# Performance work log

Hardware: AMD Instinct MI355X
Metric: run time of the kernel (lower is better)

The kernel has to match this reference:

```python
import jax, jax.numpy as jnp
import numpy as np

N, P, H = 4096, 128, 4
E = P // H           # per-head embed dim (=32)
NSEG = 32            # number of distinct position segments
NEG = -1e30          # mask fill (safe finite -inf)


def setup_inputs() -> dict:
    key = jax.random.key(0)
    ks = jax.random.split(key, 8)
    s = 1.0 / np.sqrt(P)
    return {
        "inp": jax.random.normal(ks[0], (N, P), jnp.float32),
        "pos": jax.random.randint(ks[1], (N,), 0, NSEG, jnp.int32),
        "Wq": jax.random.normal(ks[2], (P, P), jnp.float32) * s,
        "bq": jnp.zeros((P,), jnp.float32),
        "Wk": jax.random.normal(ks[3], (P, P), jnp.float32) * s,
        "bk": jnp.zeros((P,), jnp.float32),
        "Wv": jax.random.normal(ks[4], (P, P), jnp.float32) * s,
        "bv": jnp.zeros((P,), jnp.float32),
    }


def reference(inp, pos, Wq, bq, Wk, bk, Wv, bv):
    # Per-segment multi-head self-attention. The TF while_loop gathers rows of
    # each unique `pos` value, runs attention within that segment, and scatters
    # results back to the original row order. This is mathematically identical
    # to full attention with a same-segment mask (softmax restricted to keys
    # in the same segment), which is the vectorized form here.
    n = inp.shape[0]

    def heads(x, W, b):
        # (n, p) -> (h, n, e), matching rearrange 'n (h e) -> h n e'
        y = x @ W + b
        return y.reshape(n, H, E).transpose(1, 0, 2)

    q = heads(inp, Wq, bq)
    k = heads(inp, Wk, bk)
    v = heads(inp, Wv, bv)

    score = jnp.einsum('hne,hme->hnm', q, k) / np.sqrt(E).astype(np.float32)
    same_seg = (pos[:, None] == pos[None, :])[None, :, :]      # (1, n, n)
    score = jnp.where(same_seg, score, NEG)
    weight = jax.nn.softmax(score, axis=-1)                    # (h, n, n)
    out = jnp.einsum('hnm,hme->hne', weight, v)                # (h, n, e)
    # rearrange 'h n e -> n (h e)'
    return out.transpose(1, 0, 2).reshape(n, P)
```

## Files before the change

kernel.cpp:

```cpp
#include <hip/hip_runtime.h>
#include <hip/hip_bf16.h>
#include <math.h>

#define N 4096
#define P 128
#define H 4
#define E 32
#define NSEG 32
#define TPB 256
#define PROJ_TASKS 192

#define VSTRIDE 264
#define NEGF -3.0e38f

typedef __attribute__((ext_vector_type(8))) short bf16x8;
typedef __attribute__((ext_vector_type(4))) float f32x4;
typedef unsigned short u16;

__device__ __forceinline__ u16 f2b(float x) {
    __hip_bfloat16 b = __float2bfloat16(x);
    return *(u16*)&b;
}

__device__ __forceinline__ void sort_phase(const int* __restrict__ pos,
                                           int* __restrict__ seg_rows,
                                           int* __restrict__ seg_off,
                                           int* sm, int t) {
    int* cnt = sm;
    int* cur = sm + NSEG;
    int* off = sm + 2 * NSEG;
    if (t < NSEG) cnt[t] = 0;
    __syncthreads();
    for (int i = t; i < N; i += TPB) atomicAdd(&cnt[pos[i]], 1);
    __syncthreads();
    if (t == 0) {
        int s = 0;
        for (int k = 0; k < NSEG; ++k) { off[k] = s; s += cnt[k]; }
        off[NSEG] = s;
    }
    __syncthreads();
    if (t <= NSEG) seg_off[t] = off[t];
    if (t < NSEG) cur[t] = off[t];
    __syncthreads();
    for (int i = t; i < N; i += TPB) {
        int r = atomicAdd(&cur[pos[i]], 1);
        seg_rows[r] = i;
    }
}

__device__ __forceinline__ void proj_phase(int task,
                                           const float* __restrict__ x,
                                           const float* __restrict__ Wq, const float* __restrict__ bq,
                                           const float* __restrict__ Wk, const float* __restrict__ bk,
                                           const float* __restrict__ Wv, const float* __restrict__ bv,
                                           u16* __restrict__ Q, u16* __restrict__ Ko, u16* __restrict__ Vo,
                                           float* sm, int t) {
    float* Xl = sm;
    float* Wl = sm + 8192;

    const int mat = task >> 6;
    const int r0  = (task & 63) * 64;
    const float* W = (mat == 0) ? Wq : (mat == 1) ? Wk : Wv;
    const float* b = (mat == 0) ? bq : (mat == 1) ? bk : bv;
    u16* y         = (mat == 0) ? Q  : (mat == 1) ? Ko : Vo;

    for (int i = t * 4; i < 64 * 128; i += TPB * 4) {
        *(float4*)(Xl + i) = *(const float4*)(x + (size_t)r0 * 128 + i);
    }

    const int tc = t & 31;
    const int tr = t >> 5;

    float4 bb = *(const float4*)(b + tc * 4);
    float4 acc[8];
#pragma unroll
    for (int r = 0; r < 8; ++r) acc[r] = bb;

    for (int kc = 0; kc < 128; kc += 32) {
        __syncthreads();
        for (int i = t * 4; i < 32 * 128; i += TPB * 4) {
            *(float4*)(Wl + i) = *(const float4*)(W + (size_t)kc * 128 + i);
        }
        __syncthreads();
#pragma unroll
        for (int k0 = 0; k0 < 32; k0 += 4) {
            float4 w0 = *(float4*)&Wl[(k0 + 0) * 128 + tc * 4];
            float4 w1 = *(float4*)&Wl[(k0 + 1) * 128 + tc * 4];
            float4 w2 = *(float4*)&Wl[(k0 + 2) * 128 + tc * 4];
            float4 w3 = *(float4*)&Wl[(k0 + 3) * 128 + tc * 4];
#pragma unroll
            for (int r = 0; r < 8; ++r) {
                float4 xv = *(float4*)&Xl[(tr * 8 + r) * 128 + kc + k0];
                acc[r].x = fmaf(xv.x, w0.x, acc[r].x);
                acc[r].y = fmaf(xv.x, w0.y, acc[r].y);
                acc[r].z = fmaf(xv.x, w0.z, acc[r].z);
                acc[r].w = fmaf(xv.x, w0.w, acc[r].w);
                acc[r].x = fmaf(xv.y, w1.x, acc[r].x);
                acc[r].y = fmaf(xv.y, w1.y, acc[r].y);
                acc[r].z = fmaf(xv.y, w1.z, acc[r].z);
                acc[r].w = fmaf(xv.y, w1.w, acc[r].w);
                acc[r].x = fmaf(xv.z, w2.x, acc[r].x);
                acc[r].y = fmaf(xv.z, w2.y, acc[r].y);
                acc[r].z = fmaf(xv.z, w2.z, acc[r].z);
                acc[r].w = fmaf(xv.z, w2.w, acc[r].w);
                acc[r].x = fmaf(xv.w, w3.x, acc[r].x);
                acc[r].y = fmaf(xv.w, w3.y, acc[r].y);
                acc[r].z = fmaf(xv.w, w3.z, acc[r].z);
                acc[r].w = fmaf(xv.w, w3.w, acc[r].w);
            }
        }
    }

#pragma unroll
    for (int r = 0; r < 8; ++r) {
        ushort4 st;
        st.x = f2b(acc[r].x); st.y = f2b(acc[r].y);
        st.z = f2b(acc[r].z); st.w = f2b(acc[r].w);
        *(ushort4*)(y + (size_t)(r0 + tr * 8 + r) * 128 + tc * 4) = st;
    }
}

__global__ __launch_bounds__(TPB) void sort_proj_kernel(
        const float* __restrict__ inp, const int* __restrict__ pos,
        const float* __restrict__ Wq, const float* __restrict__ bq,
        const float* __restrict__ Wk, const float* __restrict__ bk,
        const float* __restrict__ Wv, const float* __restrict__ bv,
        u16* __restrict__ Q, u16* __restrict__ Kb, u16* __restrict__ Vb,
        int* __restrict__ seg_rows, int* __restrict__ seg_off) {
    __shared__ __align__(16) float sm[12288];
    const int b = blockIdx.x;
    const int t = threadIdx.x;
    if (b == 0) {
        sort_phase(pos, seg_rows, seg_off, (int*)sm, t);
    } else {
        proj_phase(b - 1, inp, Wq, bq, Wk, bk, Wv, bv, Q, Kb, Vb, sm, t);
    }
}

template <int KT>
__device__ __forceinline__ void attn_body(int beg, int len, int h, int z,
                                          const u16* __restrict__ Qb,
                                          const u16* __restrict__ Kb,
                                          const u16* __restrict__ Vb,
                                          const int* __restrict__ seg_rows,
                                          float* __restrict__ out,
                                          u16* __restrict__ smu,
                                          int t, int w, int col, int quad) {
    const float scale = 0.17677669529663687f;
    u16* Vt = smu;
    u16* Ps = smu + (32 + w * 16) * VSTRIDE;

#pragma unroll
    for (int ii = 0; ii < KT / 4; ++ii) {
        const int idx = ii * TPB + t;
        const int key = idx >> 2, c = idx & 3;
        bf16x8 v = {0, 0, 0, 0, 0, 0, 0, 0};
        if (key < len)
            v = *(const bf16x8*)(Vb + (size_t)seg_rows[beg + key] * 128 + h * 32 + c * 8);
#pragma unroll
        for (int j = 0; j < 8; ++j)
            Vt[(c * 8 + j) * VSTRIDE + key] = (u16)v[j];
    }

    const int tt = z * 4 + w;
    const bool have = (tt * 16 < len);
    float lrow[4];

    if (have) {
        const int qi = beg + min(tt * 16 + col, len - 1);
        const bf16x8 qa = *(const bf16x8*)(Qb + (size_t)seg_rows[qi] * 128 + h * 32 + quad * 8);

        int krow[KT];
#pragma unroll
        for (int kt = 0; kt < KT; ++kt)
            krow[kt] = seg_rows[beg + min(kt * 16 + col, len - 1)];

        f32x4 S[KT];
#pragma unroll
        for (int kt = 0; kt < KT; ++kt) {
            const bf16x8 kb = *(const bf16x8*)(Kb + (size_t)krow[kt] * 128 + h * 32 + quad * 8);
            f32x4 c = {0.f, 0.f, 0.f, 0.f};
            S[kt] = __builtin_amdgcn_mfma_f32_16x16x32_bf16(qa, kb, c, 0, 0, 0);
        }

        float mrow[4] = {NEGF, NEGF, NEGF, NEGF};
#pragma unroll
        for (int kt = 0; kt < KT; ++kt) {
            const bool kvalid = (kt * 16 + col) < len;
#pragma unroll
            for (int r = 0; r < 4; ++r) {
                const float sc = kvalid ? S[kt][r] * scale : NEGF;
                S[kt][r] = sc;
                mrow[r] = fmaxf(mrow[r], sc);
            }
        }
#pragma unroll
        for (int d = 1; d < 16; d <<= 1) {
#pragma unroll
            for (int r = 0; r < 4; ++r)
                mrow[r] = fmaxf(mrow[r], __shfl_xor(mrow[r], d));
        }
        lrow[0] = lrow[1] = lrow[2] = lrow[3] = 0.f;
#pragma unroll
        for (int kt = 0; kt < KT; ++kt) {
#pragma unroll
            for (int r = 0; r < 4; ++r) {
                const float p = __expf(S[kt][r] - mrow[r]);
                S[kt][r] = p;
                lrow[r] += p;
            }
        }
#pragma unroll
        for (int d = 1; d < 16; d <<= 1) {
#pragma unroll
            for (int r = 0; r < 4; ++r)
                lrow[r] += __shfl_xor(lrow[r], d);
        }
#pragma unroll
        for (int kt = 0; kt < KT; ++kt) {
#pragma unroll
            for (int r = 0; r < 4; ++r)
                Ps[(quad * 4 + r) * VSTRIDE + kt * 16 + col] = f2b(S[kt][r]);
        }
    }

    __syncthreads();

    if (have) {
        f32x4 o0 = {0.f, 0.f, 0.f, 0.f}, o1 = {0.f, 0.f, 0.f, 0.f};
#pragma unroll
        for (int kg = 0; kg < KT / 2; ++kg) {
            const bf16x8 pa = *(const bf16x8*)(Ps + col * VSTRIDE + kg * 32 + quad * 8);
            const bf16x8 v0 = *(const bf16x8*)(Vt + col * VSTRIDE + kg * 32 + quad * 8);
            const bf16x8 v1 = *(const bf16x8*)(Vt + (16 + col) * VSTRIDE + kg * 32 + quad * 8);
            o0 = __builtin_amdgcn_mfma_f32_16x16x32_bf16(pa, v0, o0, 0, 0, 0);
            o1 = __builtin_amdgcn_mfma_f32_16x16x32_bf16(pa, v1, o1, 0, 0, 0);
        }
#pragma unroll
        for (int r = 0; r < 4; ++r) {
            const int qloc = tt * 16 + quad * 4 + r;
            if (qloc < len) {
                const int orow = seg_rows[beg + qloc];
                const float inv = 1.0f / lrow[r];
                float* op = out + (size_t)orow * 128 + h * 32;
                op[col]      = o0[r] * inv;
                op[16 + col] = o1[r] * inv;
            }
        }
    }
}

__global__ __launch_bounds__(TPB) void attn_kernel(const u16* __restrict__ Qb,
                                                   const u16* __restrict__ Kb,
                                                   const u16* __restrict__ Vb,
                                                   const int* __restrict__ seg_rows,
                                                   const int* __restrict__ seg_off,
                                                   float* __restrict__ out) {
    __shared__ u16 smu[VSTRIDE * (32 + 4 * 16)];

    const int s = blockIdx.x, h = blockIdx.y, z = blockIdx.z;
    const int beg = seg_off[s];
    const int len = seg_off[s + 1] - beg;
    if (z * 64 >= len) return;
    const int t = threadIdx.x, w = t >> 6;
    const int lane = t & 63, col = lane & 15, quad = lane >> 4;

    if (len <= 128)
        attn_body<8>(beg, len, h, z, Qb, Kb, Vb, seg_rows, out, smu, t, w, col, quad);
    else
        attn_body<16>(beg, len, h, z, Qb, Kb, Vb, seg_rows, out, smu, t, w, col, quad);
}

extern "C" void kernel_launch(void* const* d_in, const int* in_sizes, int n_in,
                              void* d_out, int out_size, void* d_ws, size_t ws_size,
                              hipStream_t stream) {
    const float* inp = (const float*)d_in[0];
    const int*   pos = (const int*)d_in[1];
    const float* Wq  = (const float*)d_in[2];
    const float* bq  = (const float*)d_in[3];
    const float* Wk  = (const float*)d_in[4];
    const float* bk  = (const float*)d_in[5];
    const float* Wv  = (const float*)d_in[6];
    const float* bv  = (const float*)d_in[7];
    float* out = (float*)d_out;

    u16* Qb = (u16*)d_ws;
    u16* Kb = Qb + (size_t)N * 128;
    u16* Vb = Kb + (size_t)N * 128;
    int* seg_rows = (int*)(Vb + (size_t)N * 128);
    int* seg_off  = seg_rows + N;

    sort_proj_kernel<<<1 + PROJ_TASKS, TPB, 0, stream>>>(
        inp, pos, Wq, bq, Wk, bk, Wv, bv, Qb, Kb, Vb, seg_rows, seg_off);

    attn_kernel<<<dim3(NSEG, H, 4), TPB, 0, stream>>>(
        Qb, Kb, Vb, seg_rows, seg_off, out);
}
```

Measured before the change: 90.90 us.

## Replace whole-segment attention with per-wave online-softmax over 128-key chunks

The attention kernel now has each wave loop over keys in chunks of 128 using an online softmax (running max, sum and rescaled accumulators). Previously the block loaded the whole segment's V into shared memory and switched between 8-tile and 16-tile template paths. Each wave now stages its own copy of V and P in a private LDS region, so the block-wide __syncthreads is gone and a wave only waits on itself. The cost is that every wave reloads and transposes the same V chunk, adding redundant global and LDS traffic. It also adds the rescale arithmetic for segments longer than 128 keys.

New measurement: 93.91 us. 3.3% more time.

```diff
diff --git a/kernel.cpp b/kernel.cpp
--- a/kernel.cpp
+++ b/kernel.cpp
@@ -10,7 +10,7 @@
 #define TPB 256
 #define PROJ_TASKS 192
 
-#define VSTRIDE 264
+#define VS2 136
 #define NEGF -3.0e38f
 
 typedef __attribute__((ext_vector_type(8))) short bf16x8;
@@ -137,138 +137,135 @@
     }
 }
 
-template <int KT>
-__device__ __forceinline__ void attn_body(int beg, int len, int h, int z,
-                                          const u16* __restrict__ Qb,
-                                          const u16* __restrict__ Kb,
-                                          const u16* __restrict__ Vb,
-                                          const int* __restrict__ seg_rows,
-                                          float* __restrict__ out,
-                                          u16* __restrict__ smu,
-                                          int t, int w, int col, int quad) {
-    const float scale = 0.17677669529663687f;
-    u16* Vt = smu;
-    u16* Ps = smu + (32 + w * 16) * VSTRIDE;
-
-#pragma unroll
-    for (int ii = 0; ii < KT / 4; ++ii) {
-        const int idx = ii * TPB + t;
-        const int key = idx >> 2, c = idx & 3;
-        bf16x8 v = {0, 0, 0, 0, 0, 0, 0, 0};
-        if (key < len)
-            v = *(const bf16x8*)(Vb + (size_t)seg_rows[beg + key] * 128 + h * 32 + c * 8);
-#pragma unroll
-        for (int j = 0; j < 8; ++j)
-            Vt[(c * 8 + j) * VSTRIDE + key] = (u16)v[j];
-    }
-
-    const int tt = z * 4 + w;
-    const bool have = (tt * 16 < len);
-    float lrow[4];
-
-    if (have) {
-        const int qi = beg + min(tt * 16 + col, len - 1);
-        const bf16x8 qa = *(const bf16x8*)(Qb + (size_t)seg_rows[qi] * 128 + h * 32 + quad * 8);
-
-        int krow[KT];
-#pragma unroll
-        for (int kt = 0; kt < KT; ++kt)
-            krow[kt] = seg_rows[beg + min(kt * 16 + col, len - 1)];
-
-        f32x4 S[KT];
-#pragma unroll
-        for (int kt = 0; kt < KT; ++kt) {
-            const bf16x8 kb = *(const bf16x8*)(Kb + (size_t)krow[kt] * 128 + h * 32 + quad * 8);
-            f32x4 c = {0.f, 0.f, 0.f, 0.f};
-            S[kt] = __builtin_amdgcn_mfma_f32_16x16x32_bf16(qa, kb, c, 0, 0, 0);
-        }
-
-        float mrow[4] = {NEGF, NEGF, NEGF, NEGF};
-#pragma unroll
-        for (int kt = 0; kt < KT; ++kt) {
-            const bool kvalid = (kt * 16 + col) < len;
-#pragma unroll
-            for (int r = 0; r < 4; ++r) {
-                const float sc = kvalid ? S[kt][r] * scale : NEGF;
-                S[kt][r] = sc;
-                mrow[r] = fmaxf(mrow[r], sc);
-            }
-        }
-#pragma unroll
-        for (int d = 1; d < 16; d <<= 1) {
-#pragma unroll
-            for (int r = 0; r < 4; ++r)
-                mrow[r] = fmaxf(mrow[r], __shfl_xor(mrow[r], d));
-        }
-        lrow[0] = lrow[1] = lrow[2] = lrow[3] = 0.f;
-#pragma unroll
-        for (int kt = 0; kt < KT; ++kt) {
-#pragma unroll
-            for (int r = 0; r < 4; ++r) {
-                const float p = __expf(S[kt][r] - mrow[r]);
-                S[kt][r] = p;
-                lrow[r] += p;
-            }
-        }
-#pragma unroll
-        for (int d = 1; d < 16; d <<= 1) {
-#pragma unroll
-            for (int r = 0; r < 4; ++r)
-                lrow[r] += __shfl_xor(lrow[r], d);
-        }
-#pragma unroll
-        for (int kt = 0; kt < KT; ++kt) {
-#pragma unroll
-            for (int r = 0; r < 4; ++r)
-                Ps[(quad * 4 + r) * VSTRIDE + kt * 16 + col] = f2b(S[kt][r]);
-        }
-    }
-
-    __syncthreads();
-
-    if (have) {
-        f32x4 o0 = {0.f, 0.f, 0.f, 0.f}, o1 = {0.f, 0.f, 0.f, 0.f};
-#pragma unroll
-        for (int kg = 0; kg < KT / 2; ++kg) {
-            const bf16x8 pa = *(const bf16x8*)(Ps + col * VSTRIDE + kg * 32 + quad * 8);
-            const bf16x8 v0 = *(const bf16x8*)(Vt + col * VSTRIDE + kg * 32 + quad * 8);
-            const bf16x8 v1 = *(const bf16x8*)(Vt + (16 + col) * VSTRIDE + kg * 32 + quad * 8);
-            o0 = __builtin_amdgcn_mfma_f32_16x16x32_bf16(pa, v0, o0, 0, 0, 0);
-            o1 = __builtin_amdgcn_mfma_f32_16x16x32_bf16(pa, v1, o1, 0, 0, 0);
-        }
-#pragma unroll
-        for (int r = 0; r < 4; ++r) {
-            const int qloc = tt * 16 + quad * 4 + r;
-            if (qloc < len) {
-                const int orow = seg_rows[beg + qloc];
-                const float inv = 1.0f / lrow[r];
-                float* op = out + (size_t)orow * 128 + h * 32;
-                op[col]      = o0[r] * inv;
-                op[16 + col] = o1[r] * inv;
-            }
-        }
-    }
-}
-
 __global__ __launch_bounds__(TPB) void attn_kernel(const u16* __restrict__ Qb,
                                                    const u16* __restrict__ Kb,
                                                    const u16* __restrict__ Vb,
                                                    const int* __restrict__ seg_rows,
                                                    const int* __restrict__ seg_off,
                                                    float* __restrict__ out) {
-    __shared__ u16 smu[VSTRIDE * (32 + 4 * 16)];
+    __shared__ u16 smu[4 * 48 * VS2];
 
     const int s = blockIdx.x, h = blockIdx.y, z = blockIdx.z;
     const int beg = seg_off[s];
     const int len = seg_off[s + 1] - beg;
-    if (z * 64 >= len) return;
     const int t = threadIdx.x, w = t >> 6;
     const int lane = t & 63, col = lane & 15, quad = lane >> 4;
-
-    if (len <= 128)
-        attn_body<8>(beg, len, h, z, Qb, Kb, Vb, seg_rows, out, smu, t, w, col, quad);
-    else
-        attn_body<16>(beg, len, h, z, Qb, Kb, Vb, seg_rows, out, smu, t, w, col, quad);
+    const int tt = z * 4 + w;
+    if (tt * 16 >= len) return;
+    const float scale = 0.17677669529663687f;
+
+    u16* Vt = smu + w * 48 * VS2;
+    u16* Ps = Vt + 32 * VS2;
+
+    const int qi = beg + min(tt * 16 + col, len - 1);
+    const bf16x8 qa = *(const bf16x8*)(Qb + (size_t)seg_rows[qi] * 128 + h * 32 + quad * 8);
+
+    float m[4] = {NEGF, NEGF, NEGF, NEGF};
+    float l[4] = {0.f, 0.f, 0.f, 0.f};
+    f32x4 o0 = {0.f, 0.f, 0.f, 0.f}, o1 = {0.f, 0.f, 0.f, 0.f};
+
+    for (int c0 = 0; c0 < len; c0 += 128) {
+        const int cl = min(128, len - c0);
+
+#pragma unroll
+        for (int it = 0; it < 8; ++it) {
+            const int idx = it * 64 + lane;
+            const int key = idx >> 2, c = idx & 3;
+            bf16x8 v = {0, 0, 0, 0, 0, 0, 0, 0};
+            if (c0 + key < len)
+                v = *(const bf16x8*)(Vb + (size_t)seg_rows[beg + c0 + key] * 128 + h * 32 + c * 8);
+#pragma unroll
+            for (int j = 0; j < 8; ++j)
+                Vt[(c * 8 + j) * VS2 + key] = (u16)v[j];
+        }
+
+        int krow[8];
+#pragma unroll
+        for (int kt = 0; kt < 8; ++kt)
+            krow[kt] = seg_rows[beg + min(c0 + kt * 16 + col, len - 1)];
+
+        f32x4 S[8];
+#pragma unroll
+        for (int kt = 0; kt < 8; ++kt) {
+            const bf16x8 kb = *(const bf16x8*)(Kb + (size_t)krow[kt] * 128 + h * 32 + quad * 8);
+            f32x4 c4 = {0.f, 0.f, 0.f, 0.f};
+            S[kt] = __builtin_amdgcn_mfma_f32_16x16x32_bf16(qa, kb, c4, 0, 0, 0);
+        }
+
+        float mc[4] = {NEGF, NEGF, NEGF, NEGF};
+#pragma unroll
+        for (int kt = 0; kt < 8; ++kt) {
+            const bool kv = (kt * 16 + col) < cl;
+#pragma unroll
+            for (int r = 0; r < 4; ++r) {
+                const float sc = kv ? S[kt][r] * scale : NEGF;
+                S[kt][r] = sc;
+                mc[r] = fmaxf(mc[r], sc);
+            }
+        }
+#pragma unroll
+        for (int d = 1; d < 16; d <<= 1) {
+#pragma unroll
+            for (int r = 0; r < 4; ++r)
+                mc[r] = fmaxf(mc[r], __shfl_xor(mc[r], d));
+        }
+        float corr[4];
+#pragma unroll
+        for (int r = 0; r < 4; ++r) {
+            const float mn = fmaxf(m[r], mc[r]);
+            corr[r] = __expf(m[r] - mn);
+            m[r] = mn;
+        }
+        float lc[4] = {0.f, 0.f, 0.f, 0.f};
+#pragma unroll
+        for (int kt = 0; kt < 8; ++kt) {
+#pragma unroll
+            for (int r = 0; r < 4; ++r) {
+                const float p = __expf(S[kt][r] - m[r]);
+                S[kt][r] = p;
+                lc[r] += p;
+            }
+        }
+#pragma unroll
+        for (int d = 1; d < 16; d <<= 1) {
+#pragma unroll
+            for (int r = 0; r < 4; ++r)
+                lc[r] += __shfl_xor(lc[r], d);
+        }
+#pragma unroll
+        for (int r = 0; r < 4; ++r) {
+            l[r] = l[r] * corr[r] + lc[r];
+            o0[r] *= corr[r];
+            o1[r] *= corr[r];
+        }
+
+#pragma unroll
+        for (int kt = 0; kt < 8; ++kt) {
+#pragma unroll
+            for (int r = 0; r < 4; ++r)
+                Ps[(quad * 4 + r) * VS2 + kt * 16 + col] = f2b(S[kt][r]);
+        }
+#pragma unroll
+        for (int kg = 0; kg < 4; ++kg) {
+            const bf16x8 pa = *(const bf16x8*)(Ps + col * VS2 + kg * 32 + quad * 8);
+            const bf16x8 v0 = *(const bf16x8*)(Vt + col * VS2 + kg * 32 + quad * 8);
+            const bf16x8 v1 = *(const bf16x8*)(Vt + (16 + col) * VS2 + kg * 32 + quad * 8);
+            o0 = __builtin_amdgcn_mfma_f32_16x16x32_bf16(pa, v0, o0, 0, 0, 0);
+            o1 = __builtin_amdgcn_mfma_f32_16x16x32_bf16(pa, v1, o1, 0, 0, 0);
+        }
+    }
+
+#pragma unroll
+    for (int r = 0; r < 4; ++r) {
+        const int qloc = tt * 16 + quad * 4 + r;
+        if (qloc < len) {
+            const int orow = seg_rows[beg + qloc];
+            const float inv = 1.0f / l[r];
+            float* op = out + (size_t)orow * 128 + h * 32;
+            op[col]      = o0[r] * inv;
+            op[16 + col] = o1[r] * inv;
+        }
+    }
 }
 
 extern "C" void kernel_launch(void* const* d_in, const int* in_sizes, int n_in,
```
